# Performance work log

Hardware: AMD Instinct MI355X
Metric: run time of the kernel (lower is better)

The kernel has to match this reference:

```python
import jax, jax.numpy as jnp
import numpy as np

# SSD post-process constants (mirror torch module init args)
V0, V1 = 0.1, 0.2            # box coder variances
SCORE_THRESH = 0.05
NMS_THRESH = 0.45
DET_PER_IMG = 100
MIN_SIZE = 0.01
PRE_NMS_TOPK = 1000          # padded candidate budget for jit-safe NMS


def setup_inputs() -> dict:
    key = jax.random.key(0)
    k1, k2, k3 = jax.random.split(key, 3)
    B, P, C = 32, 24564, 81
    pred_logits = jax.random.normal(k1, (B, P, C), dtype=jnp.float32)
    pred_boxes = jax.random.normal(k2, (B, P, 4), dtype=jnp.float32)
    # priors in (cx, cy, w, h), normalized coords
    u = jax.random.uniform(k3, (P, 4), dtype=jnp.float32)
    priors = jnp.concatenate([u[:, :2], 0.02 + 0.3 * u[:, 2:]], axis=-1)
    target_sizes = 512.0 * jnp.ones((B, 2), dtype=jnp.float32)  # (h, w)
    return {"pred_logits": pred_logits, "pred_boxes": pred_boxes,
            "priors": priors, "target_sizes": target_sizes}


def _decode(rel, priors):
    # SSD box decode: priors are cxcywh, rel codes scaled by variances -> xyxy
    xy = priors[:, :2] + rel[:, :2] * V0 * priors[:, 2:]
    wh = priors[:, 2:] * jnp.exp(rel[:, 2:] * V1)
    return jnp.concatenate([xy - wh / 2, xy + wh / 2], axis=-1)


def _box_iou(a, b):
    area_a = (a[:, 2] - a[:, 0]) * (a[:, 3] - a[:, 1])
    area_b = (b[:, 2] - b[:, 0]) * (b[:, 3] - b[:, 1])
    lt = jnp.maximum(a[:, None, :2], b[None, :, :2])
    rb = jnp.minimum(a[:, None, 2:], b[None, :, 2:])
    wh = jnp.clip(rb - lt, 0.0)
    inter = wh[..., 0] * wh[..., 1]
    return inter / (area_a[:, None] + area_b[None, :] - inter + 1e-12)


def _per_image(logits, rel, priors, tsize):
    P, C = logits.shape
    boxes = _decode(rel, priors)                       # [P,4] xyxy
    scale = jnp.tile(tsize[::-1], 2)                   # (w,h,w,h) = flip(0).repeat(2)
    boxes = boxes * scale
    scores = jax.nn.softmax(logits, axis=-1)[:, 1:]    # drop background, [P,C-1]
    size_ok = ((boxes[:, 2] - boxes[:, 0]) >= MIN_SIZE) & \
              ((boxes[:, 3] - boxes[:, 1]) >= MIN_SIZE)
    masked = jnp.where((scores > SCORE_THRESH) & size_ok[:, None], scores, -1.0)
    top_s, top_i = jax.lax.top_k(masked.reshape(-1), PRE_NMS_TOPK)
    prior_i = top_i // (C - 1)
    cls0 = top_i % (C - 1)                             # label - 1
    b = boxes[prior_i]                                 # [K,4]
    valid = top_s > SCORE_THRESH
    # batched_nms: offset boxes by class so different classes never overlap
    maxc = jnp.max(jnp.where(valid[:, None], b, 0.0))
    bo = b + (cls0.astype(b.dtype) * (maxc + 1.0))[:, None]
    ious = jax.lax.stop_gradient(_box_iou(bo, bo))
    K = PRE_NMS_TOPK
    idx = jnp.arange(K)

    def body(i, keep):
        sup = jnp.any(keep & (idx < i) & (ious[i] > NMS_THRESH))
        return keep.at[i].set(keep[i] & ~sup)

    keep = jax.lax.fori_loop(0, K, body, valid)
    kept_s = jnp.where(keep, top_s, -1.0)
    fs, fi = jax.lax.top_k(kept_s, DET_PER_IMG)        # keep order == score order
    fb = b[fi]
    fl = cls0[fi] + 1
    fvalid = fs > SCORE_THRESH
    fb = jnp.where(fvalid[:, None], fb, 0.0)
    fl = jnp.where(fvalid, fl, -1)
    fs = jnp.where(fvalid, fs, 0.0)
    return fb, fs, fl, fvalid


def reference(pred_logits, pred_boxes, priors, target_sizes):
    # Returns padded per-image detections: boxes [B,100,4], scores [B,100],
    # labels [B,100] (int, -1 = padding), valid mask [B,100].
    return jax.vmap(_per_image, in_axes=(0, 0, None, 0))(
        pred_logits, pred_boxes, priors, target_sizes)
```

## Files before the change

kernel.cpp:

```cpp
#include <hip/hip_runtime.h>
#include <stdint.h>

typedef unsigned int u32;
typedef unsigned long long u64;
typedef long long i64;

#define NCLS 81
#define KTOP 1000
#define DETS 100
#define CANDCAP 2048
#define BIGCAP 131072
#define TPB 256
#define RCH 64
#define NCH 4
#define CNT_STRIDE 32
#define FBINS 4096

__device__ __forceinline__ double fast_exp(double x)
{
    const double LOG2E = 1.4426950408889634074;
    const double LN2HI = 6.93147180369123816490e-01;
    const double LN2LO = 1.90821492927058770002e-10;
    double nf = rint(x * LOG2E);
    int n = (int)nf;
    double r = fma(-nf, LN2HI, x);
    r = fma(-nf, LN2LO, r);
    double p = 2.7557319223985893e-06;
    p = fma(p, r, 2.4801587301587302e-05);
    p = fma(p, r, 1.9841269841269841e-04);
    p = fma(p, r, 1.3888888888888889e-03);
    p = fma(p, r, 8.3333333333333332e-03);
    p = fma(p, r, 4.1666666666666664e-02);
    p = fma(p, r, 1.6666666666666666e-01);
    p = fma(p, r, 5.0000000000000000e-01);
    p = fma(p, r, 1.0);
    p = fma(p, r, 1.0);
    i64 bits = ((i64)(n + 1023)) << 52;
    return p * __longlong_as_double(bits);
}

__global__ __launch_bounds__(TPB, 7)
void score_kernel(const float* __restrict__ logits, const float* __restrict__ rel,
                  const float* __restrict__ priors, const float* __restrict__ ts,
                  int P, u64* __restrict__ bigCand, u32* __restrict__ bigCnt)
{
    __shared__ float xs[RCH * NCLS];
    __shared__ double sden[RCH];
    __shared__ float tfl[RCH];
    __shared__ u32 okm[RCH];
    __shared__ u32 wsum[4];
    __shared__ u32 s_base;
    int img = blockIdx.y;
    int p0 = blockIdx.x * TPB;
    int tid = threadIdx.x;
    int lane = tid & 63, wid = tid >> 6;
    int sub = tid & 3;
    int rloc = tid >> 2;

    for (int ch = 0; ch < NCH; ++ch) {
        int rbase = p0 + ch * RCH;
        __syncthreads();
        int nrows = min(RCH, P - rbase);
        if (nrows == RCH) {
            const float4* s4 = (const float4*)(logits + ((size_t)img * P + rbase) * NCLS);
            float4* d4 = (float4*)xs;
#pragma unroll
            for (int k = 0; k < 5; ++k) d4[k * TPB + tid] = s4[k * TPB + tid];
            if (tid < 16) d4[5 * TPB + tid] = s4[5 * TPB + tid];
        } else if (nrows > 0) {
            const float* s1 = logits + ((size_t)img * P + rbase) * NCLS;
            int nflat = nrows * NCLS;
            for (int f = tid; f < nflat; f += TPB) xs[f] = s1[f];
        }
        __syncthreads();

        int p = rbase + rloc;
        bool live = (p < P);
        const float* row = xs + rloc * NCLS;

        float vals[21];
#pragma unroll
        for (int i = 0; i < 21; ++i) {
            int j = sub + 4 * i;
            vals[i] = (live && j < NCLS) ? row[j] : -1.0e30f;
        }

        float m = vals[0];
#pragma unroll
        for (int i = 1; i < 21; ++i) m = fmaxf(m, vals[i]);
        m = fmaxf(m, __shfl_xor(m, 1));
        m = fmaxf(m, __shfl_xor(m, 2));

        double md = (double)m;
        double acc = 0.0;
#pragma unroll
        for (int i = 0; i < 21; ++i) {
            if (vals[i] > -1.0e29f)
                acc += fast_exp((double)vals[i] - md);
        }
        acc += __shfl_xor(acc, 1);
        acc += __shfl_xor(acc, 2);
        double s = acc;
        if (sub == 0) sden[rloc] = s;
        __syncthreads();

        if (tid < RCH) {
            int p2 = rbase + tid;
            bool ok2 = false;
            float t2 = 3.4e38f;
            if (p2 < P) {
                double s2 = sden[tid];
                t2 = logf(0.05f * (float)s2) - 3e-4f;
                const float* rp = rel + ((size_t)img * P + p2) * 4;
                const float* pp = priors + (size_t)p2 * 4;
                double pw = pp[2], ph = pp[3];
                double cx = (double)pp[0] + (double)rp[0] * 0.1 * pw;
                double cy = (double)pp[1] + (double)rp[1] * 0.1 * ph;
                double bw = pw * fast_exp((double)rp[2] * 0.2);
                double bh = ph * fast_exp((double)rp[3] * 0.2);
                double sw = (double)ts[img * 2 + 1], sh = (double)ts[img * 2 + 0];
                double x1 = (cx - bw * 0.5) * sw, x2 = (cx + bw * 0.5) * sw;
                double y1 = (cy - bh * 0.5) * sh, y2 = (cy + bh * 0.5) * sh;
                ok2 = (x2 - x1 >= 0.01) && (y2 - y1 >= 0.01);
            }
            okm[tid] = ok2 ? 1u : 0u;
            tfl[tid] = t2;
        }
        __syncthreads();
        bool ok = okm[rloc] != 0;
        float tf_lo = tfl[rloc];

        u32 cnt = 0;
#pragma unroll
        for (int i = 0; i < 21; ++i) {
            int j = sub + 4 * i;
            if (ok && j != 0 && vals[i] - m > tf_lo) cnt++;
        }
        u32 inc = cnt;
        for (int off = 1; off < 64; off <<= 1) {
            u32 v = __shfl_up(inc, off);
            if (lane >= off) inc += v;
        }
        if (lane == 63) wsum[wid] = inc;
        __syncthreads();
        if (tid == 0) {
            u32 tot = wsum[0] + wsum[1] + wsum[2] + wsum[3];
            s_base = tot ? atomicAdd(&bigCnt[(size_t)img * CNT_STRIDE], tot) : 0u;
        }
        __syncthreads();
        if (ok && cnt) {
            u32 wbase = 0;
            for (int w = 0; w < wid; ++w) wbase += wsum[w];
            u32 pos = s_base + wbase + inc - cnt;
#pragma unroll
            for (int i = 0; i < 21; ++i) {
                int j = sub + 4 * i;
                if (j != 0 && vals[i] - m > tf_lo) {
                    double e = fast_exp((double)vals[i] - md);
                    double sc = e / s;
                    u64 entry = 0ULL;
                    if (sc > 0.05) {
                        u32 key = __float_as_uint((float)sc) ^ 0x80000000u;
                        u32 idx = (u32)p * 80u + (u32)(j - 1);
                        entry = ((u64)key << 32) | (u64)(u32)(~idx);
                    }
                    if (pos < BIGCAP)
                        bigCand[(size_t)img * BIGCAP + pos] = entry;
                    pos++;
                }
            }
        }
    }
}

__global__ __launch_bounds__(1024)
void select_nms_kernel(const u64* __restrict__ bigCand, const u32* __restrict__ bigCnt,
                       const float* __restrict__ rel, const float* __restrict__ priors,
                       const float* __restrict__ ts, int P,
                       float* __restrict__ out, int B)
{
    __shared__ u64 smemU[7584];
    __shared__ u64 supW16[16];
    __shared__ u32 s_sel, s_run, s_floor, s_cnt;
    __shared__ int s_i;
    int img = blockIdx.x;
    int tid = threadIdx.x;
    int lane = tid & 63;
    int wv = tid >> 6;
    u32 bc = bigCnt[(size_t)img * CNT_STRIDE];
    if (bc > (u32)BIGCAP) bc = BIGCAP;
    const u64* src = bigCand + (size_t)img * BIGCAP;

    u64* s = smemU;
    u32* h = (u32*)((char*)smemU + 16384);

    for (int i = tid; i < FBINS; i += 1024) h[i] = 0;
    if (tid == 0) s_cnt = 0;
    __syncthreads();
    for (u32 k = tid; k < bc; k += 1024) {
        u32 key = (u32)(src[k] >> 32);
        if (key) atomicAdd(&h[key >> 20], 1u);
    }
    __syncthreads();
    if (tid == 0) {
        u32 run = 0; int d = FBINS - 1;
        for (; d >= 0; --d) {
            if (run + h[d] >= KTOP) break;
            run += h[d];
        }
        s_sel = (u32)d;
        s_run = run;
    }
    __syncthreads();
    u32 d12 = s_sel;
    if ((int)d12 >= 0) {
        u32 run0 = s_run;
        if (tid < 16) h[tid] = 0;
        __syncthreads();
        for (u32 k = tid; k < bc; k += 1024) {
            u32 key = (u32)(src[k] >> 32);
            if (key && (key >> 20) == d12) atomicAdd(&h[(key >> 16) & 0xF], 1u);
        }
        __syncthreads();
        if (tid == 0) {
            u32 run = run0;
            int b = 15;
            for (; b >= 0; --b) {
                run += h[b];
                if (run >= KTOP) break;
            }
            if (b < 0) b = 0;
            s_floor = ((d12 << 4) | (u32)b) << 16;
        }
    } else {
        if (tid == 0) s_floor = 0u;
    }
    __syncthreads();
    u32 fkey = s_floor;
    for (u32 k0 = 0; k0 < bc; k0 += 1024) {
        u32 k = k0 + tid;
        u64 e = 0; bool pass = false;
        if (k < bc) {
            e = src[k];
            u32 ky = (u32)(e >> 32);
            pass = ky && (ky >= fkey);
        }
        u64 mask = __ballot(pass);
        if (mask) {
            int leader = __ffsll((long long)mask) - 1;
            u32 basePos = 0;
            if (lane == leader) basePos = atomicAdd(&s_cnt, (u32)__popcll(mask));
            basePos = __shfl(basePos, leader);
            if (pass) {
                u32 pos = basePos + (u32)__popcll(mask & ((1ULL << lane) - 1ULL));
                if (pos < CANDCAP) s[pos] = e;
            }
        }
    }
    __syncthreads();
    u32 n = s_cnt; if (n > CANDCAP) n = CANDCAP;
    for (int k = tid; k < CANDCAP; k += 1024)
        if ((u32)k >= n) s[k] = 0ULL;
    __syncthreads();
    for (u32 len = 2; len <= CANDCAP; len <<= 1) {
        for (u32 j = len >> 1; j > 0; j >>= 1) {
            for (int i = tid; i < CANDCAP; i += 1024) {
                u32 ixj = (u32)i ^ j;
                if (ixj > (u32)i) {
                    u64 a = s[i], b = s[ixj];
                    bool up = ((i & len) == 0);
                    if (up ? (a < b) : (a > b)) { s[i] = b; s[ixj] = a; }
                }
            }
            __syncthreads();
        }
    }

    u64 e = (tid < KTOP) ? s[tid] : 0ULL;
    __syncthreads();

    double* o0   = (double*)smemU;
    double* o1   = (double*)((char*)smemU +  8000);
    double* o2   = (double*)((char*)smemU + 16000);
    double* o3   = (double*)((char*)smemU + 24000);
    double* arA  = (double*)((char*)smemU + 32000);
    int*    clsA = (int*)   ((char*)smemU + 44000);
    float*  scA  = (float*) ((char*)smemU + 48000);
    int*    keptS= (int*)   ((char*)smemU + 52000);
    double* red  = (double*)((char*)smemU + 52416);

    double b0 = 0, b1 = 0, b2 = 0, b3 = 0;
    int cls = 0;
    float score = -1.0f;
    bool validE = (tid < KTOP) && ((e >> 32) != 0ULL);
    double v = -1e300;
    if (tid < KTOP) {
        if (validE) {
            u32 key = (u32)(e >> 32);
            score = __uint_as_float(key ^ 0x80000000u);
            u32 idx = ~((u32)e);
            int p = (int)(idx / 80u), c0 = (int)(idx % 80u);
            cls = c0;
            const float* rp = rel + ((size_t)img * P + p) * 4;
            const float* pp = priors + (size_t)p * 4;
            double pw = pp[2], ph = pp[3];
            double cx = (double)pp[0] + (double)rp[0] * 0.1 * pw;
            double cy = (double)pp[1] + (double)rp[1] * 0.1 * ph;
            double bw = pw * fast_exp((double)rp[2] * 0.2);
            double bh = ph * fast_exp((double)rp[3] * 0.2);
            double sw = (double)ts[img * 2 + 1], sh = (double)ts[img * 2 + 0];
            b0 = (cx - bw * 0.5) * sw; b1 = (cy - bh * 0.5) * sh;
            b2 = (cx + bw * 0.5) * sw; b3 = (cy + bh * 0.5) * sh;
            v = fmax(fmax(b0, b1), fmax(b2, b3));
        } else {
            v = 0.0;
        }
        o0[tid] = b0; o1[tid] = b1; o2[tid] = b2; o3[tid] = b3;
        clsA[tid] = cls; scA[tid] = score;
        red[tid] = v;
    } else {
        red[tid] = -1e300;
    }
    __syncthreads();
    for (int off = 512; off > 0; off >>= 1) {
        if (tid < off) red[tid] = fmax(red[tid], red[tid + off]);
        __syncthreads();
    }
    double maxc1 = red[0] + 1.0;
    if (tid < KTOP) {
        double off_ = (double)cls * maxc1;
        double a0 = b0 + off_, a1 = b1 + off_, a2 = b2 + off_, a3 = b3 + off_;
        arA[tid] = (a2 - a0) * (a3 - a1);
    }
    u64 wb = __ballot(validE);
    if (lane == 0) supW16[wv] = wb;
    __syncthreads();
    u64 aliveW = (tid < 16) ? supW16[tid] : 0ULL;

    int cnt = 0;
    while (cnt < DETS) {
        if (wv == 0) {
            bool has = (lane < 16) && (aliveW != 0ULL);
            u64 bal = __ballot(has);
            int ni = -1;
            if (bal) {
                int w0 = __ffsll((i64)bal) - 1;
                u64 word = __shfl(aliveW, w0);
                int bt = __ffsll((i64)word) - 1;
                ni = w0 * 64 + bt;
            }
            if (lane == 0) s_i = ni;
        }
        __syncthreads();
        int i = s_i;
        if (i < 0) break;
        if (tid == 0) keptS[cnt] = i;
        cnt++;
        double offi = (double)clsA[i] * maxc1;
        double a0 = o0[i] + offi, a1 = o1[i] + offi;
        double a2 = o2[i] + offi, a3 = o3[i] + offi;
        double aA = arA[i];
        bool sup = false;
        if (tid < KTOP && tid > i) {
            double offj = (double)clsA[tid] * maxc1;
            double c0 = o0[tid] + offj, c1 = o1[tid] + offj;
            double c2 = o2[tid] + offj, c3 = o3[tid] + offj;
            double ltx = fmax(a0, c0), lty = fmax(a1, c1);
            double rbx = fmin(a2, c2), rby = fmin(a3, c3);
            double wx = fmax(rbx - ltx, 0.0), wy = fmax(rby - lty, 0.0);
            double inter = wx * wy;
            sup = inter > 0.45 * (((aA + arA[tid]) - inter) + 1e-12);
        }
        u64 ws = __ballot(sup);
        if (lane == 0) supW16[wv] = ws;
        __syncthreads();
        if (tid < 16) {
            aliveW &= ~supW16[tid];
            if (tid == (i >> 6)) aliveW &= ~(1ULL << (i & 63));
        }
    }
    __syncthreads();

    int r = tid;
    if (r < DETS) {
        float f0 = 0.f, f1 = 0.f, f2 = 0.f, f3 = 0.f, sc = 0.f, lb = -1.0f, vd = 0.f;
        if (r < cnt) {
            int i2 = keptS[r];
            f0 = (float)o0[i2]; f1 = (float)o1[i2];
            f2 = (float)o2[i2]; f3 = (float)o3[i2];
            sc = scA[i2];
            lb = (float)(clsA[i2] + 1);
            vd = 1.0f;
        }
        ((float4*)out)[(size_t)img * DETS + r] = make_float4(f0, f1, f2, f3);
        out[(size_t)B * 400 + (size_t)img * DETS + r] = sc;
        out[(size_t)B * 500 + (size_t)img * DETS + r] = lb;
        out[(size_t)B * 600 + (size_t)img * DETS + r] = vd;
    }
}

extern "C" void kernel_launch(void* const* d_in, const int* in_sizes, int n_in,
                              void* d_out, int out_size, void* d_ws, size_t ws_size,
                              hipStream_t stream)
{
    const float* logits = (const float*)d_in[0];
    const float* rel    = (const float*)d_in[1];
    const float* priors = (const float*)d_in[2];
    const float* ts     = (const float*)d_in[3];
    float* out = (float*)d_out;
    int P = in_sizes[2] / 4;
    int B = in_sizes[3] / 2;

    char* ws = (char*)d_ws;
    size_t zero_bytes = (size_t)B * CNT_STRIDE * 4;
    size_t o_big = (zero_bytes + 255) & ~(size_t)255;

    u32* bigCnt  = (u32*)ws;
    u64* bigCand = (u64*)(ws + o_big);

    hipMemsetAsync(ws, 0, zero_bytes, stream);

    dim3 g1((P + TPB - 1) / TPB, B);
    score_kernel<<<g1, TPB, 0, stream>>>(logits, rel, priors, ts, P, bigCand, bigCnt);
    select_nms_kernel<<<B, 1024, 0, stream>>>(bigCand, bigCnt, rel, priors, ts, P,
                                              out, B);
    (void)n_in; (void)out_size; (void)ws_size;
}
```

Measured before the change: 352.3 us.

## Use table-driven double exp in scoring and parallelize histogram threshold scan

Replaces the degree-11 polynomial double exp in the score kernel with a 32-entry shared-memory table plus a short degree-4 polynomial, cutting FP64 FMA work per logit. The select kernel's serial 4096-bin threshold scan by one thread becomes a block-wide suffix scan, with a short serial search inside the chosen 4-bin group. Launch bounds occupancy drops from 7 to 6 waves to give the scorer more registers. The reference exp gains extra polynomial terms for accuracy, and the table lookup adds LDS traffic and a small accuracy risk near the threshold comparisons.

```diff
diff --git a/kernel.cpp b/kernel.cpp
--- a/kernel.cpp
+++ b/kernel.cpp
@@ -16,7 +16,7 @@
 #define CNT_STRIDE 32
 #define FBINS 4096
 
-__device__ __forceinline__ double fast_exp(double x)
+__device__ __forceinline__ double exp_ref(double x)
 {
     const double LOG2E = 1.4426950408889634074;
     const double LN2HI = 6.93147180369123816490e-01;
@@ -25,7 +25,10 @@
     int n = (int)nf;
     double r = fma(-nf, LN2HI, x);
     r = fma(-nf, LN2LO, r);
-    double p = 2.7557319223985893e-06;
+    double p = 2.0876756987868099e-09;
+    p = fma(p, r, 2.5052108385441720e-08);
+    p = fma(p, r, 2.7557319223985891e-07);
+    p = fma(p, r, 2.7557319223985893e-06);
     p = fma(p, r, 2.4801587301587302e-05);
     p = fma(p, r, 1.9841269841269841e-04);
     p = fma(p, r, 1.3888888888888889e-03);
@@ -39,12 +42,32 @@
     return p * __longlong_as_double(bits);
 }
 
-__global__ __launch_bounds__(TPB, 7)
+__device__ __forceinline__ double fexp(double x, const double* __restrict__ etab)
+{
+    const double L32     = 1.4426950408889634074 * 32.0;
+    const double LN32HI  = 6.93147180369123816490e-01 / 32.0;
+    const double LN32LO  = 1.90821492927058770002e-10 / 32.0;
+    double nf = rint(x * L32);
+    int n = (int)nf;
+    double r = fma(-nf, LN32HI, x);
+    r = fma(-nf, LN32LO, r);
+    double p = 4.1666666666666664e-02;
+    p = fma(p, r, 1.6666666666666666e-01);
+    p = fma(p, r, 5.0000000000000000e-01);
+    p = fma(p, r, 1.0);
+    p = fma(p, r, 1.0);
+    double tb = etab[n & 31];
+    i64 q = (i64)(n >> 5) + 1023;
+    return (p * tb) * __longlong_as_double(q << 52);
+}
+
+__global__ __launch_bounds__(TPB, 6)
 void score_kernel(const float* __restrict__ logits, const float* __restrict__ rel,
                   const float* __restrict__ priors, const float* __restrict__ ts,
                   int P, u64* __restrict__ bigCand, u32* __restrict__ bigCnt)
 {
     __shared__ float xs[RCH * NCLS];
+    __shared__ double etab[32];
     __shared__ double sden[RCH];
     __shared__ float tfl[RCH];
     __shared__ u32 okm[RCH];
@@ -57,6 +80,9 @@
     int sub = tid & 3;
     int rloc = tid >> 2;
 
+    if (tid < 32)
+        etab[tid] = exp_ref((double)tid * (6.93147180369123816490e-01 / 32.0));
+
     for (int ch = 0; ch < NCH; ++ch) {
         int rbase = p0 + ch * RCH;
         __syncthreads();
@@ -96,7 +122,7 @@
 #pragma unroll
         for (int i = 0; i < 21; ++i) {
             if (vals[i] > -1.0e29f)
-                acc += fast_exp((double)vals[i] - md);
+                acc += fexp((double)vals[i] - md, etab);
         }
         acc += __shfl_xor(acc, 1);
         acc += __shfl_xor(acc, 2);
@@ -116,8 +142,8 @@
                 double pw = pp[2], ph = pp[3];
                 double cx = (double)pp[0] + (double)rp[0] * 0.1 * pw;
                 double cy = (double)pp[1] + (double)rp[1] * 0.1 * ph;
-                double bw = pw * fast_exp((double)rp[2] * 0.2);
-                double bh = ph * fast_exp((double)rp[3] * 0.2);
+                double bw = pw * fexp((double)rp[2] * 0.2, etab);
+                double bh = ph * fexp((double)rp[3] * 0.2, etab);
                 double sw = (double)ts[img * 2 + 1], sh = (double)ts[img * 2 + 0];
                 double x1 = (cx - bw * 0.5) * sw, x2 = (cx + bw * 0.5) * sw;
                 double y1 = (cy - bh * 0.5) * sh, y2 = (cy + bh * 0.5) * sh;
@@ -156,7 +182,7 @@
             for (int i = 0; i < 21; ++i) {
                 int j = sub + 4 * i;
                 if (j != 0 && vals[i] - m > tf_lo) {
-                    double e = fast_exp((double)vals[i] - md);
+                    double e = fexp((double)vals[i] - md, etab);
                     double sc = e / s;
                     u64 entry = 0ULL;
                     if (sc > 0.05) {
@@ -182,7 +208,7 @@
     __shared__ u64 smemU[7584];
     __shared__ u64 supW16[16];
     __shared__ u32 s_sel, s_run, s_floor, s_cnt;
-    __shared__ int s_i;
+    __shared__ int s_i, s_t;
     int img = blockIdx.x;
     int tid = threadIdx.x;
     int lane = tid & 63;
@@ -191,25 +217,42 @@
     if (bc > (u32)BIGCAP) bc = BIGCAP;
     const u64* src = bigCand + (size_t)img * BIGCAP;
 
-    u64* s = smemU;
-    u32* h = (u32*)((char*)smemU + 16384);
+    u64* s    = smemU;
+    u32* h    = (u32*)((char*)smemU + 16384);
+    u32* tsum = (u32*)((char*)smemU + 32768);
 
     for (int i = tid; i < FBINS; i += 1024) h[i] = 0;
-    if (tid == 0) s_cnt = 0;
+    if (tid == 0) { s_cnt = 0; s_t = -1; }
     __syncthreads();
     for (u32 k = tid; k < bc; k += 1024) {
         u32 key = (u32)(src[k] >> 32);
         if (key) atomicAdd(&h[key >> 20], 1u);
     }
     __syncthreads();
-    if (tid == 0) {
-        u32 run = 0; int d = FBINS - 1;
-        for (; d >= 0; --d) {
-            if (run + h[d] >= KTOP) break;
-            run += h[d];
-        }
-        s_sel = (u32)d;
-        s_run = run;
+    tsum[tid] = h[tid * 4] + h[tid * 4 + 1] + h[tid * 4 + 2] + h[tid * 4 + 3];
+    __syncthreads();
+    for (int off = 1; off < 1024; off <<= 1) {
+        u32 v = (tid + off < 1024) ? tsum[tid + off] : 0u;
+        __syncthreads();
+        tsum[tid] += v;
+        __syncthreads();
+    }
+    if (tsum[tid] >= KTOP) atomicMax(&s_t, tid);
+    __syncthreads();
+    int t_star = s_t;
+    if (t_star >= 0) {
+        if (tid == t_star) {
+            u32 run = (t_star + 1 < 1024) ? tsum[t_star + 1] : 0u;
+            int d = 4 * t_star + 3;
+            for (; d >= 4 * t_star; --d) {
+                if (run + h[d] >= KTOP) break;
+                run += h[d];
+            }
+            s_sel = (u32)d;
+            s_run = run;
+        }
+    } else {
+        if (tid == 0) s_sel = 0xFFFFFFFFu;
     }
     __syncthreads();
     u32 d12 = s_sel;
@@ -306,8 +349,8 @@
             double pw = pp[2], ph = pp[3];
             double cx = (double)pp[0] + (double)rp[0] * 0.1 * pw;
             double cy = (double)pp[1] + (double)rp[1] * 0.1 * ph;
-            double bw = pw * fast_exp((double)rp[2] * 0.2);
-            double bh = ph * fast_exp((double)rp[3] * 0.2);
+            double bw = pw * exp_ref((double)rp[2] * 0.2);
+            double bh = ph * exp_ref((double)rp[3] * 0.2);
             double sw = (double)ts[img * 2 + 1], sh = (double)ts[img * 2 + 0];
             b0 = (cx - bw * 0.5) * sw; b1 = (cy - bh * 0.5) * sh;
             b2 = (cx + bw * 0.5) * sw; b3 = (cy + bh * 0.5) * sh;
```

Result: faster. 287.0 us, median of 2 (-18.5%).
